# Performance work log

Measured on AMD Instinct MI355X. Metric: run time of the kernel, lower is better.

The kernel has to match this reference:

```python
import jax, jax.numpy as jnp
from jax import lax
import numpy as np

WINDOW_SIZES = (1, 2, 3)


def _proj(x, w1, b1, w2, b2):
    # gated projection: sigmoid(Linear1) * tanh(Linear2)
    return jax.nn.sigmoid(x @ w1.T + b1) * jnp.tanh(x @ w2.T + b2)


def setup_inputs() -> dict:
    key = jax.random.key(0)
    ks = jax.random.split(key, 16)
    V, E, D = 50000, 1024, 1024
    N, La, Lq = 64, 512, 64
    s = 0.02  # weight scale to keep sigmoid/tanh unsaturated
    return {
        "data_q": jax.random.randint(ks[0], (Lq,), 0, V),
        "data_as": jax.random.randint(ks[1], (N, La), 0, V),
        "emb": jax.random.normal(ks[2], (V, E), jnp.float32),
        "w1": jax.random.normal(ks[3], (D, E), jnp.float32) * s,
        "b1": jnp.zeros((D,), jnp.float32),
        "w2": jax.random.normal(ks[4], (D, E), jnp.float32) * s,
        "b2": jnp.zeros((D,), jnp.float32),
        "cw1": jax.random.normal(ks[5], (D, D, 1), jnp.float32) * s,
        "cb1": jnp.zeros((D,), jnp.float32),
        "cw2": jax.random.normal(ks[6], (D, D, 2), jnp.float32) * s,
        "cb2": jnp.zeros((D,), jnp.float32),
        "cw3": jax.random.normal(ks[7], (D, D, 3), jnp.float32) * s,
        "cb3": jnp.zeros((D,), jnp.float32),
        "lin_w": jax.random.normal(ks[8], (D, 3 * D), jnp.float32) * s,
        "lin_b": jnp.zeros((D,), jnp.float32),
        "soft_w": jax.random.normal(ks[9], (1, D), jnp.float32) * s,
        "soft_b": jnp.zeros((1,), jnp.float32),
    }


def reference(data_q, data_as, emb, w1, b1, w2, b2,
              cw1, cb1, cw2, cb2, cw3, cb3, lin_w, lin_b, soft_w, soft_b):
    N, La = data_as.shape
    a_tok = data_as.reshape(-1)                     # [T] concatenated answers
    emb_a = emb[a_tok]                              # [T, E]
    emb_q = emb[data_q]                             # [Lq, E]
    pa = _proj(emb_a, w1, b1, w2, b2)               # [T, D]
    pq = _proj(emb_q, w1, b1, w2, b2)               # [Lq, D]

    # attention: M_r = q @ a^T ; alpha = softmax over question positions
    M = pq @ pa.T                                   # [Lq, T]
    alpha = jax.nn.softmax(M.T, axis=1)             # [T, Lq]
    Y = alpha @ pq                                  # [T, D]
    sim = pa * Y                                    # elementwise compare (mul)

    starts = jnp.arange(N) * La
    x = sim.T[None]                                 # [1, D, T]
    pools = []
    for w, cw, cb in zip(WINDOW_SIZES, (cw1, cw2, cw3), (cb1, cb2, cb3)):
        conv = lax.conv_general_dilated(
            x, cw, (1,), 'VALID',
            dimension_numbers=('NCW', 'OIW', 'NCW'))[0].T + cb  # [T-w+1, D]
        conv = jax.nn.relu(conv)
        # DMax: per-answer max over rows [start_k, start_k + La - w + 1)
        idx = starts[:, None] + jnp.arange(La - w + 1)[None, :]  # [N, La-w+1]
        pools.append(conv[idx].max(axis=1))          # [N, D]

    cat = jnp.concatenate(pools, axis=1)            # [N, 3D]
    h = jnp.tanh(cat @ lin_w.T + lin_b)             # [N, D]
    logits = (h @ soft_w.T + soft_b).reshape(-1)    # [N]
    return jax.nn.log_softmax(logits)
```

## Files before the change

### kernel.cpp

```cpp
#include <hip/hip_runtime.h>

#define DEV __device__ __forceinline__

typedef __bf16 bf16x8 __attribute__((ext_vector_type(8)));
typedef float f32x4 __attribute__((ext_vector_type(4)));
typedef unsigned short u16;
typedef u16 u16x4 __attribute__((ext_vector_type(4)));

constexpr int T_ANS = 32768;
constexpr int LQ    = 64;
constexpr int M_ALL = T_ANS + LQ;
constexpr int M_PAD = 33024;
constexpr int DIM   = 1024;

DEV u16 f2bf(float x) {
  unsigned u = __float_as_uint(x);
  return (u16)((u + 0x7FFFu + ((u >> 16) & 1u)) >> 16);
}
DEV float bf2f(u16 s) { return __uint_as_float(((unsigned)s) << 16); }

DEV void gl2lds16(const void* g, void* l) {
  __builtin_amdgcn_global_load_lds(
      (const __attribute__((address_space(1))) unsigned int*)g,
      (__attribute__((address_space(3))) unsigned int*)l, 16, 0, 0);
}

#define MF(A, B, C) __builtin_amdgcn_mfma_f32_16x16x32_bf16(A, B, C, 0, 0, 0)
#define LFC(P, OFF) (*(const bf16x8*)((P) + (OFF)))


#define STG(G, LT, R0) gl2lds16((G) + (R0) * 2048 + gOff, (LT) + (R0) * 64 + ldOff)

#define S_TILE(AT, BT, BUF)                                                           \
  { const char* ga_ = (AT); const char* gb_ = (BT); char* lb_ = (BUF);                \
    STG(ga_, lb_, 0); STG(ga_, lb_, 128);                                             \
    STG(gb_, lb_ + 16384, 0); STG(gb_, lb_ + 16384, 128); }

#define VMC4 asm volatile("s_waitcnt vmcnt(4)" ::: "memory");
#define VMC0 asm volatile("s_waitcnt vmcnt(0)" ::: "memory");

#define TILEV3(BUF, STAGES, WAIT)                                                     \
  {                                                                                   \
    STAGES                                                                            \
    const char* Ar = (BUF) + rdA;                                                     \
    const char* Br = (BUF) + 16384 + rdB;                                             \
    bf16x8 a0 = LFC(Ar, 0),    a1 = LFC(Ar, 1024), a2 = LFC(Ar, 2048), a3 = LFC(Ar, 3072); \
    bf16x8 a4 = LFC(Ar, 4096), a5 = LFC(Ar, 5120), a6 = LFC(Ar, 6144), a7 = LFC(Ar, 7168); \
    bf16x8 c0 = LFC(Br, 0), c1 = LFC(Br, 1024), c2 = LFC(Br, 2048), c3 = LFC(Br, 3072);    \
    acc[0][0] = MF(a0, c0, acc[0][0]); acc[0][1] = MF(a0, c1, acc[0][1]);             \
    acc[0][2] = MF(a0, c2, acc[0][2]); acc[0][3] = MF(a0, c3, acc[0][3]);             \
    acc[1][0] = MF(a1, c0, acc[1][0]); acc[1][1] = MF(a1, c1, acc[1][1]);             \
    acc[1][2] = MF(a1, c2, acc[1][2]); acc[1][3] = MF(a1, c3, acc[1][3]);             \
    acc[2][0] = MF(a2, c0, acc[2][0]); acc[2][1] = MF(a2, c1, acc[2][1]);             \
    acc[2][2] = MF(a2, c2, acc[2][2]); acc[2][3] = MF(a2, c3, acc[2][3]);             \
    acc[3][0] = MF(a3, c0, acc[3][0]); acc[3][1] = MF(a3, c1, acc[3][1]);             \
    acc[3][2] = MF(a3, c2, acc[3][2]); acc[3][3] = MF(a3, c3, acc[3][3]);             \
    acc[4][0] = MF(a4, c0, acc[4][0]); acc[4][1] = MF(a4, c1, acc[4][1]);             \
    acc[4][2] = MF(a4, c2, acc[4][2]); acc[4][3] = MF(a4, c3, acc[4][3]);             \
    acc[5][0] = MF(a5, c0, acc[5][0]); acc[5][1] = MF(a5, c1, acc[5][1]);             \
    acc[5][2] = MF(a5, c2, acc[5][2]); acc[5][3] = MF(a5, c3, acc[5][3]);             \
    acc[6][0] = MF(a6, c0, acc[6][0]); acc[6][1] = MF(a6, c1, acc[6][1]);             \
    acc[6][2] = MF(a6, c2, acc[6][2]); acc[6][3] = MF(a6, c3, acc[6][3]);             \
    acc[7][0] = MF(a7, c0, acc[7][0]); acc[7][1] = MF(a7, c1, acc[7][1]);             \
    acc[7][2] = MF(a7, c2, acc[7][2]); acc[7][3] = MF(a7, c3, acc[7][3]);             \
    WAIT                                                                              \
    asm volatile("s_barrier" ::: "memory");                                           \
  }

#define CORE_BASES                                                                    \
  const int ldOff = tid * 16;                                                         \
  const int gOff = (tid >> 2) * 2048 + (((tid & 3) ^ ((tid >> 2) & 3)) << 4);         \
  const int blk_ = (((lane >> 4) ^ (lane & 3)) << 4);                                 \
  const int rdA = (wm + (lane & 15)) * 64 + blk_;                                     \
  const int rdB = (wn + (lane & 15)) * 64 + blk_;                                     \
  char* b0_ = lds; char* b1_ = lds + 32768; char* b2_ = lds + 65536; char* b3_ = lds + 98304;

#define GROUP4(T0)                                                                    \
    TILEV3(b0_, S_TILE(Ab((T0) + 2), Bb((T0) + 2), b2_), VMC4)                        \
    TILEV3(b1_, S_TILE(Ab((T0) + 3), Bb((T0) + 3), b3_), VMC4)                        \
    TILEV3(b2_, S_TILE(Ab((T0) + 4), Bb((T0) + 4), b0_), VMC4)                        \
    TILEV3(b3_, S_TILE(Ab((T0) + 5), Bb((T0) + 5), b1_), VMC4)


__global__ __launch_bounds__(256)
void prep_all(const float* __restrict__ w1, const float* __restrict__ w2,
              u16* __restrict__ W12,
              const float* __restrict__ lin_w, u16* __restrict__ linb,
              const float* __restrict__ cw1, const float* __restrict__ cw2,
              const float* __restrict__ cw3, u16* __restrict__ cwb,
              float* __restrict__ cat,
              const int* __restrict__ dq, const int* __restrict__ das,
              const float* __restrict__ emb, u16* __restrict__ X) {
  const int b = blockIdx.x, t = threadIdx.x;
  if (b < 8192) {
    int i = b * 256 + t;
    int n2 = i >> 10, k = i & 1023;
    int j = n2 >> 4, m = n2 & 15;
    const float* src = (j & 1) ? w2 : w1;
    W12[i] = f2bf(src[(size_t)((j >> 1) * 16 + m) * 1024 + k]);
  } else if (b < 11264) {
    int i = (b - 8192) * 256 + t;
    float4 v = ((const float4*)lin_w)[i];
    u16x4 o = { f2bf(v.x), f2bf(v.y), f2bf(v.z), f2bf(v.w) };
    ((u16x4*)linb)[i] = o;
  } else if (b < 23552) {
    int rb = b - 11264;
    int W = 1 + (rb >> 12);
    int i = (rb & 4095) * 256 + t;
    const float* src = (W == 1) ? cw1 : (W == 2) ? cw2 : cw3;
    u16* dst = cwb + ((W == 1) ? 0 : (W == 2) ? (size_t)1 * 1048576 : (size_t)3 * 1048576);
#pragma unroll 3
    for (int k = 0; k < 3; ++k)
      if (k < W)
        dst[(size_t)k * 1048576 + i] = f2bf(src[(size_t)i * W + k]);
  } else if (b < 24320) {
    cat[(b - 23552) * 256 + t] = 0.f;
  } else {
    const int row = b - 24320;
    size_t dsto = (size_t)row * DIM + t * 4;
    if (row >= M_ALL) {
      u16x4 z = {0, 0, 0, 0};
      *(u16x4*)(X + dsto) = z;
      return;
    }
    const int tok = (row < T_ANS) ? das[row] : dq[row - T_ANS];
    float4 v = ((const float4*)(emb + (size_t)tok * DIM))[t];
    u16x4 o = { f2bf(v.x), f2bf(v.y), f2bf(v.z), f2bf(v.w) };
    *(u16x4*)(X + dsto) = o;
  }
}

__global__ void transpose_pq(const u16* __restrict__ pa, u16* __restrict__ pqT) {
  int i = blockIdx.x * 256 + threadIdx.x;
  int e = i >> 6, q = i & 63;
  pqT[i] = pa[(size_t)(T_ANS + q) * DIM + e];
}

__global__ void zero_pad_sim(u16* __restrict__ sim) {
  int i = blockIdx.x * 256 + threadIdx.x;
  if (i < 2 * DIM) sim[(size_t)T_ANS * DIM + i] = 0;
}

__global__ void cast_cat(const float* __restrict__ cat, u16* __restrict__ catb) {
  int i = blockIdx.x * 256 + threadIdx.x;
  if (i < 128 * 3072) {
    int row = i / 3072;
    catb[i] = (row < 64) ? f2bf(cat[i]) : (u16)0;
  }
}


__global__ __launch_bounds__(256)
void proj_g(const u16* __restrict__ X, const u16* __restrict__ W12,
            const float* __restrict__ b1, const float* __restrict__ b2,
            u16* __restrict__ pa) {
  __shared__ alignas(16) u16 sA[128 * 32];
  __shared__ alignas(16) u16 sB[128 * 32];
  const int tid = threadIdx.x, lane = tid & 63;
  const int wid = tid >> 6;
  const int wm = (wid >> 1) * 64, wn = (wid & 1) * 64;
  const int wg = ((int)blockIdx.x % 8) * 516 + (int)blockIdx.x / 8;
  const int tm = (wg >> 4) * 128, tn = (wg & 15) * 128;
  f32x4 acc[4][4] = {};
  for (int k0 = 0; k0 < 1024; k0 += 32) {
#pragma unroll
    for (int j = 0; j < 2; ++j) {
      const int f = tid * 16 + j * 4096;
      const int r = f >> 6, cb = f & 63;
      gl2lds16((const char*)X   + (size_t)(tm + r) * 2048 + k0 * 2 + cb, (char*)sA + f);
      gl2lds16((const char*)W12 + (size_t)(tn + r) * 2048 + k0 * 2 + cb, (char*)sB + f);
    }
    __syncthreads();
    const int lr = lane & 15, lk = (lane >> 4) * 8;
    bf16x8 af[4], bf[4];
#pragma unroll
    for (int i = 0; i < 4; ++i) {
      af[i] = *(const bf16x8*)(sA + (wm + i * 16 + lr) * 32 + lk);
      bf[i] = *(const bf16x8*)(sB + (wn + i * 16 + lr) * 32 + lk);
    }
#pragma unroll
    for (int mi = 0; mi < 4; ++mi)
#pragma unroll
      for (int ni = 0; ni < 4; ++ni)
        acc[mi][ni] = MF(af[mi], bf[ni], acc[mi][ni]);
    __syncthreads();
  }
  const int lr = lane & 15, lg = (lane >> 4) * 4;
#pragma unroll
  for (int np = 0; np < 2; ++np) {
    const int col = ((tn + wn) >> 1) + np * 16 + lr;
    const float b1v = b1[col], b2v = b2[col];
#pragma unroll
    for (int mi = 0; mi < 4; ++mi)
#pragma unroll
      for (int r = 0; r < 4; ++r) {
        const int row = tm + wm + mi * 16 + lg + r;
        const float x1 = acc[mi][2 * np][r] + b1v;
        const float x2 = acc[mi][2 * np + 1][r] + b2v;
        const float sg = 1.f / (1.f + __expf(-x1));
        const float th = 2.f / (1.f + __expf(-2.f * x2)) - 1.f;
        pa[(size_t)row * DIM + col] = f2bf(sg * th);
      }
  }
}


__global__ __launch_bounds__(512, 1)
void conv_fused(const u16* __restrict__ sim, const u16* __restrict__ cwb,
                const float* __restrict__ cb1, const float* __restrict__ cb2,
                const float* __restrict__ cb3, float* __restrict__ cat) {
  extern __shared__ char lds[];
  const int tid = threadIdx.x, lane = tid & 63;
  const int wid = tid >> 6;
  const int wm = (wid >> 2) * 128, wn = (wid & 3) * 64;
  const int lr = lane & 15;
  const int wg = ((int)blockIdx.x % 8) * 64 + (int)blockIdx.x / 8;
  const int tm = (wg >> 2) * 256, tn = (wg & 3) * 256;
  const char* Ag = (const char*)sim + (size_t)tm * 2048;
  const char* Bg = (const char*)cwb + (size_t)tn * 2048;
  auto Ab = [&](int t) {
    const int g = t >> 5;
    const int tap = g - (g > 0) - 2 * (g > 2);
    return Ag + tap * 2048 + ((t & 31) << 6);
  };
  auto Bb = [&](int t) { return Bg + (size_t)(t >> 5) * 2097152 + ((t & 31) << 6); };

  f32x4 acc[8][4] = {};
  CORE_BASES

  const int lg = (lane >> 4) * 4;
  const int n = tm >> 9;
  auto epi = [&](int W, const float* cb, int outoff) {
#pragma unroll
    for (int ni = 0; ni < 4; ++ni) {
      const int col = tn + wn + ni * 16 + lr;
      const float cbv = cb[col];
      float vmax = 0.f;
#pragma unroll
      for (int mi = 0; mi < 8; ++mi)
#pragma unroll
        for (int r = 0; r < 4; ++r) {
          const int t = tm + wm + mi * 16 + lg + r;
          float v = fmaxf(acc[mi][ni][r] + cbv, 0.f);
          if ((t & 511) > 512 - W) v = 0.f;
          vmax = fmaxf(vmax, v);
        }
      vmax = fmaxf(vmax, __shfl_xor(vmax, 16));
      vmax = fmaxf(vmax, __shfl_xor(vmax, 32));
      if (lane < 16)
        atomicMax((int*)&cat[(size_t)n * 3072 + outoff + col], __float_as_int(vmax));
    }
#pragma unroll
    for (int i = 0; i < 8; ++i)
#pragma unroll
      for (int j = 0; j < 4; ++j) acc[i][j] = (f32x4){0.f, 0.f, 0.f, 0.f};
  };

  S_TILE(Ab(0), Bb(0), b0_) S_TILE(Ab(1), Bb(1), b1_)
  VMC4
  asm volatile("s_barrier" ::: "memory");
  for (int g = 0; g < 8; ++g) { GROUP4(4 * g) }
  epi(1, cb1, 0);
  for (int g = 8; g < 24; ++g) { GROUP4(4 * g) }
  epi(2, cb2, 1024);
  for (int g = 24; g < 47; ++g) { GROUP4(4 * g) }
  {
    TILEV3(b0_, S_TILE(Ab(190), Bb(190), b2_), VMC4)
    TILEV3(b1_, S_TILE(Ab(191), Bb(191), b3_), VMC4)
    TILEV3(b2_, , VMC0)
    TILEV3(b3_, , )
  }
  epi(3, cb3, 2048);
}


__global__ __launch_bounds__(256, 2)
void attn_s(const u16* __restrict__ pa, float* __restrict__ Spart) {
  __shared__ alignas(16) u16 sA[128 * 32];
  __shared__ alignas(16) u16 sB[64 * 32];
  const int tid = threadIdx.x, lane = tid & 63;
  const int tm = blockIdx.x * 128;
  const int kbase = blockIdx.y * 256;
  const int wid = tid >> 6;
  const int wm = (wid >> 1) * 64, wn = (wid & 1) * 32;
  const u16* pq = pa + (size_t)T_ANS * DIM;
  f32x4 acc[4][2] = {};
  for (int k0 = kbase; k0 < kbase + 256; k0 += 32) {
#pragma unroll
    for (int j = 0; j < 2; ++j) {
      const int f = tid * 16 + j * 4096;
      const int r = f >> 6, cb = f & 63;
      gl2lds16((const char*)pa + (size_t)(tm + r) * 2048 + k0 * 2 + cb, (char*)sA + f);
    }
    {
      const int f = tid * 16;
      const int r = f >> 6, cb = f & 63;
      gl2lds16((const char*)pq + (size_t)r * 2048 + k0 * 2 + cb, (char*)sB + f);
    }
    __syncthreads();
    const int lr = lane & 15, lk = (lane >> 4) * 8;
    bf16x8 af[4], bfr[2];
#pragma unroll
    for (int i = 0; i < 4; ++i)
      af[i] = *(const bf16x8*)(sA + (wm + i * 16 + lr) * 32 + lk);
#pragma unroll
    for (int i = 0; i < 2; ++i)
      bfr[i] = *(const bf16x8*)(sB + (wn + i * 16 + lr) * 32 + lk);
#pragma unroll
    for (int mi = 0; mi < 4; ++mi)
#pragma unroll
      for (int ni = 0; ni < 2; ++ni)
        acc[mi][ni] = MF(af[mi], bfr[ni], acc[mi][ni]);
    __syncthreads();
  }
  const int lr = lane & 15, lg = (lane >> 4) * 4;
  float* Sp = Spart + (size_t)blockIdx.y * (T_ANS * 64);
#pragma unroll
  for (int mi = 0; mi < 4; ++mi)
#pragma unroll
    for (int ni = 0; ni < 2; ++ni)
#pragma unroll
      for (int r = 0; r < 4; ++r) {
        const int row = tm + wm + mi * 16 + lg + r;
        const int col = wn + ni * 16 + lr;
        Sp[(size_t)row * 64 + col] = acc[mi][ni][r];
      }
}

__global__ void softmax64(const float* __restrict__ Spart, u16* __restrict__ alpha) {
  const int row = blockIdx.x * 4 + (threadIdx.x >> 6);
  const int lane = threadIdx.x & 63;
  const size_t o = (size_t)row * 64 + lane;
  float v = Spart[o] + Spart[(size_t)1 * T_ANS * 64 + o]
          + Spart[(size_t)2 * T_ANS * 64 + o] + Spart[(size_t)3 * T_ANS * 64 + o];
  float m = v;
#pragma unroll
  for (int o2 = 32; o2 > 0; o2 >>= 1) m = fmaxf(m, __shfl_xor(m, o2));
  const float e = __expf(v - m);
  float s = e;
#pragma unroll
  for (int o2 = 32; o2 > 0; o2 >>= 1) s += __shfl_xor(s, o2);
  alpha[(size_t)row * 64 + lane] = f2bf(e / s);
}


__global__ __launch_bounds__(256, 2)
void attn_y_sim(const u16* __restrict__ alpha, const u16* __restrict__ pqT,
                const u16* __restrict__ pa, u16* __restrict__ sim) {
  __shared__ alignas(16) u16 sA[128 * 32];
  __shared__ alignas(16) u16 sB[128 * 32];
  const int tid = threadIdx.x, lane = tid & 63;
  const int tm = blockIdx.x * 128, tn = blockIdx.y * 128;
  const int wid = tid >> 6;
  const int wm = (wid >> 1) * 64, wn = (wid & 1) * 64;
  f32x4 acc[4][4] = {};
  for (int k0 = 0; k0 < 64; k0 += 32) {
#pragma unroll
    for (int j = 0; j < 2; ++j) {
      const int f = tid * 16 + j * 4096;
      const int r = f >> 6, cb = f & 63;
      gl2lds16((const char*)alpha + (size_t)(tm + r) * 128 + k0 * 2 + cb, (char*)sA + f);
      gl2lds16((const char*)pqT   + (size_t)(tn + r) * 128 + k0 * 2 + cb, (char*)sB + f);
    }
    __syncthreads();
    const int lr = lane & 15, lk = (lane >> 4) * 8;
    bf16x8 af[4], bfr[4];
#pragma unroll
    for (int i = 0; i < 4; ++i) {
      af[i]  = *(const bf16x8*)(sA + (wm + i * 16 + lr) * 32 + lk);
      bfr[i] = *(const bf16x8*)(sB + (wn + i * 16 + lr) * 32 + lk);
    }
#pragma unroll
    for (int mi = 0; mi < 4; ++mi)
#pragma unroll
      for (int ni = 0; ni < 4; ++ni)
        acc[mi][ni] = MF(af[mi], bfr[ni], acc[mi][ni]);
    __syncthreads();
  }
  const int lr = lane & 15, lg = (lane >> 4) * 4;
#pragma unroll
  for (int ni = 0; ni < 4; ++ni) {
    const int col = tn + wn + ni * 16 + lr;
#pragma unroll
    for (int mi = 0; mi < 4; ++mi)
#pragma unroll
      for (int r = 0; r < 4; ++r) {
        const int row = tm + wm + mi * 16 + lg + r;
        const size_t o = (size_t)row * DIM + col;
        sim[o] = f2bf(bf2f(pa[o]) * acc[mi][ni][r]);
      }
  }
}


__global__ __launch_bounds__(256, 2)
void final_h(const u16* __restrict__ catb, const u16* __restrict__ linb,
             const float* __restrict__ lin_b, float* __restrict__ h) {
  __shared__ alignas(16) u16 sA[128 * 32];
  __shared__ alignas(16) u16 sB[128 * 32];
  const int tid = threadIdx.x, lane = tid & 63;
  const int tn = blockIdx.y * 128;
  const int wid = tid >> 6;
  const int wm = (wid >> 1) * 64, wn = (wid & 1) * 64;
  f32x4 acc[4][4] = {};
  for (int k0 = 0; k0 < 3072; k0 += 32) {
#pragma unroll
    for (int j = 0; j < 2; ++j) {
      const int f = tid * 16 + j * 4096;
      const int r = f >> 6, cb = f & 63;
      gl2lds16((const char*)catb + (size_t)r * 6144 + k0 * 2 + cb, (char*)sA + f);
      gl2lds16((const char*)linb + (size_t)(tn + r) * 6144 + k0 * 2 + cb, (char*)sB + f);
    }
    __syncthreads();
    const int lr = lane & 15, lk = (lane >> 4) * 8;
    bf16x8 af[4], bfr[4];
#pragma unroll
    for (int i = 0; i < 4; ++i) {
      af[i]  = *(const bf16x8*)(sA + (wm + i * 16 + lr) * 32 + lk);
      bfr[i] = *(const bf16x8*)(sB + (wn + i * 16 + lr) * 32 + lk);
    }
#pragma unroll
    for (int mi = 0; mi < 4; ++mi)
#pragma unroll
      for (int ni = 0; ni < 4; ++ni)
        acc[mi][ni] = MF(af[mi], bfr[ni], acc[mi][ni]);
    __syncthreads();
  }
  const int lr = lane & 15, lg = (lane >> 4) * 4;
#pragma unroll
  for (int ni = 0; ni < 4; ++ni) {
    const int col = tn + wn + ni * 16 + lr;
    const float bv = lin_b[col];
#pragma unroll
    for (int mi = 0; mi < 4; ++mi)
#pragma unroll
      for (int r = 0; r < 4; ++r) {
        const int row = wm + mi * 16 + lg + r;
        if (row < 64) {
          const float x = acc[mi][ni][r] + bv;
          h[(size_t)row * DIM + col] = 2.f / (1.f + __expf(-2.f * x)) - 1.f;
        }
      }
  }
}

__global__ void final_logits(const float* __restrict__ h, const float* __restrict__ soft_w,
                             const float* __restrict__ soft_b, float* __restrict__ out) {
  __shared__ float part[256];
  const int t = threadIdx.x;
  const int n = t >> 2, q = t & 3;
  float s = 0.f;
  for (int j = q * 256; j < q * 256 + 256; ++j) s += h[(size_t)n * DIM + j] * soft_w[j];
  part[t] = s;
  __syncthreads();
  if (t < 64) {
    float logit = part[t * 4] + part[t * 4 + 1] + part[t * 4 + 2] + part[t * 4 + 3] + soft_b[0];
    float m = logit;
#pragma unroll
    for (int o = 32; o > 0; o >>= 1) m = fmaxf(m, __shfl_xor(m, o));
    float e = __expf(logit - m);
    float ssum = e;
#pragma unroll
    for (int o = 32; o > 0; o >>= 1) ssum += __shfl_xor(ssum, o);
    out[t] = (logit - m) - logf(ssum);
  }
}


extern "C" void kernel_launch(void* const* d_in, const int* in_sizes, int n_in,
                              void* d_out, int out_size, void* d_ws, size_t ws_size,
                              hipStream_t stream) {
  const int*   data_q  = (const int*)d_in[0];
  const int*   data_as = (const int*)d_in[1];
  const float* emb     = (const float*)d_in[2];
  const float* w1      = (const float*)d_in[3];
  const float* b1      = (const float*)d_in[4];
  const float* w2      = (const float*)d_in[5];
  const float* b2      = (const float*)d_in[6];
  const float* cw1     = (const float*)d_in[7];
  const float* cb1     = (const float*)d_in[8];
  const float* cw2     = (const float*)d_in[9];
  const float* cb2     = (const float*)d_in[10];
  const float* cw3     = (const float*)d_in[11];
  const float* cb3     = (const float*)d_in[12];
  const float* lin_w   = (const float*)d_in[13];
  const float* lin_b   = (const float*)d_in[14];
  const float* soft_w  = (const float*)d_in[15];
  const float* soft_b  = (const float*)d_in[16];
  float* out = (float*)d_out;

  hipFuncSetAttribute((const void*)conv_fused, hipFuncAttributeMaxDynamicSharedMemorySize, 131072);

  u16* X     = (u16*)d_ws;
  u16* pa    = X    + (size_t)M_PAD * DIM;
  u16* W12   = pa   + (size_t)M_PAD * DIM;
  u16* cwb   = W12  + (size_t)2 * 1024 * 1024;
  u16* linb  = cwb  + (size_t)6 * 1024 * 1024;
  u16* pqT   = linb + (size_t)3 * 1024 * 1024;
  u16* alpha = pqT  + 64 * 1024;
  float* cat = (float*)(alpha + (size_t)T_ANS * 64);
  u16* catb  = (u16*)(cat + 64 * 3072);
  float* h   = (float*)(catb + 128 * 3072);
  u16* simb  = X;
  float* Spart = (float*)X;

  prep_all<<<57344, 256, 0, stream>>>(w1, w2, W12, lin_w, linb, cw1, cw2, cw3, cwb,
                                      cat, data_q, data_as, emb, X);

  proj_g<<<4128, 256, 0, stream>>>(X, W12, b1, b2, pa);
  transpose_pq<<<256, 256, 0, stream>>>(pa, pqT);

  attn_s<<<dim3(T_ANS / 128, 4), 256, 0, stream>>>(pa, Spart);
  softmax64<<<T_ANS / 4, 256, 0, stream>>>(Spart, alpha);
  attn_y_sim<<<dim3(T_ANS / 128, 8), 256, 0, stream>>>(alpha, pqT, pa, simb);
  zero_pad_sim<<<8, 256, 0, stream>>>(simb);

  conv_fused<<<512, 512, 131072, stream>>>(simb, cwb, cb1, cb2, cb3, cat);

  cast_cat<<<1536, 256, 0, stream>>>(cat, catb);
  final_h<<<dim3(1, 8), 256, 0, stream>>>(catb, linb, lin_b, h);
  final_logits<<<1, 256, 0, stream>>>(h, soft_w, soft_b, out);
}
```

Baseline: 736.6 us.

## Rewrite projection GEMM as persistent 256-row tiles with 4-stage LDS pipeline

The gated projection GEMM for answer tokens is rebuilt to reuse the conv kernel's deep pipelined MFMA core. It launches 256 persistent 512-thread blocks that each own 256 rows and sweep four 128-wide column segments (w1 and w2 interleaved), running the sigmoid*tanh epilogue after each segment. The question rows get their own small kernel. The LDS swizzle is also changed, which affects the shared conv kernel too. This is meant to raise MFMA utilization and A-tile reuse over the old 128x128 tile kernel, at the cost of fewer blocks and higher register pressure.

New measurement: 895.4 us. 1.22x slower.

```diff
diff --git a/kernel.cpp b/kernel.cpp
--- a/kernel.cpp
+++ b/kernel.cpp
@@ -69,8 +69,8 @@
 
 #define CORE_BASES                                                                    \
   const int ldOff = tid * 16;                                                         \
-  const int gOff = (tid >> 2) * 2048 + (((tid & 3) ^ ((tid >> 2) & 3)) << 4);         \
-  const int blk_ = (((lane >> 4) ^ (lane & 3)) << 4);                                 \
+  const int gOff = (tid >> 2) * 2048 + (((tid & 3) ^ ((tid >> 3) & 3)) << 4);         \
+  const int blk_ = (((lane >> 4) ^ ((lane >> 1) & 3)) << 4);                          \
   const int rdA = (wm + (lane & 15)) * 64 + blk_;                                     \
   const int rdB = (wn + (lane & 15)) * 64 + blk_;                                     \
   char* b0_ = lds; char* b1_ = lds + 32768; char* b2_ = lds + 65536; char* b3_ = lds + 98304;
@@ -150,17 +150,81 @@
 }
 
 
-__global__ __launch_bounds__(256)
+__global__ __launch_bounds__(512, 1)
 void proj_g(const u16* __restrict__ X, const u16* __restrict__ W12,
             const float* __restrict__ b1, const float* __restrict__ b2,
             u16* __restrict__ pa) {
+  extern __shared__ char lds[];
+  const int tid = threadIdx.x, lane = tid & 63;
+  const int wid = tid >> 6;
+  const int wm = (wid >> 2) * 128, wn = (wid & 3) * 64;
+  const int lr = lane & 15, lg = (lane >> 4) * 4;
+  const int wg = ((int)blockIdx.x % 8) * 32 + (int)blockIdx.x / 8;
+  const int tm = (wg & 127) * 256, tnh = wg >> 7;
+  const char* Ag = (const char*)X + (size_t)tm * 2048;
+  const char* Bg = (const char*)W12 + (size_t)tnh * 2097152;
+  auto Ab = [&](int t) { return Ag + ((t & 31) << 6); };
+  auto Bb = [&](int t) { return Bg + (size_t)(t >> 5) * 524288 + ((t & 31) << 6); };
+
+  f32x4 acc[8][4] = {};
+  CORE_BASES
+
+  auto epi = [&](int seg) {
+    const int colbase = (tnh * 4 + seg) * 128;
+#pragma unroll
+    for (int pp = 0; pp < 2; ++pp) {
+      const int clocal = ((wn >> 5) + pp) * 16 + lr;
+      const int col = colbase + clocal;
+      const float b1v = b1[col], b2v = b2[col];
+#pragma unroll
+      for (int mi = 0; mi < 8; ++mi)
+#pragma unroll
+        for (int r = 0; r < 4; ++r) {
+          const int row = tm + wm + mi * 16 + lg + r;
+          const float x1 = acc[mi][2 * pp][r] + b1v;
+          const float x2 = acc[mi][2 * pp + 1][r] + b2v;
+          const float sg = 1.f / (1.f + __expf(-x1));
+          const float th = 2.f / (1.f + __expf(-2.f * x2)) - 1.f;
+          pa[(size_t)row * DIM + col] = f2bf(sg * th);
+        }
+    }
+#pragma unroll
+    for (int i = 0; i < 8; ++i)
+#pragma unroll
+      for (int j = 0; j < 4; ++j) acc[i][j] = (f32x4){0.f, 0.f, 0.f, 0.f};
+  };
+
+  S_TILE(Ab(0), Bb(0), b0_) S_TILE(Ab(1), Bb(1), b1_)
+  VMC4
+  asm volatile("s_barrier" ::: "memory");
+  for (int g = 0; g < 8; ++g) { GROUP4(4 * g) }
+  epi(0);
+  for (int g = 8; g < 16; ++g) { GROUP4(4 * g) }
+  epi(1);
+  for (int g = 16; g < 24; ++g) { GROUP4(4 * g) }
+  epi(2);
+  for (int g = 24; g < 31; ++g) { GROUP4(4 * g) }
+  {
+    TILEV3(b0_, S_TILE(Ab(126), Bb(126), b2_), VMC4)
+    TILEV3(b1_, S_TILE(Ab(127), Bb(127), b3_), VMC4)
+    TILEV3(b2_, , VMC0)
+    TILEV3(b3_, , )
+  }
+  epi(3);
+}
+
+
+__global__ __launch_bounds__(256)
+void proj_pq(const u16* __restrict__ X, const u16* __restrict__ W12,
+             const float* __restrict__ b1, const float* __restrict__ b2,
+             u16* __restrict__ pa) {
   __shared__ alignas(16) u16 sA[128 * 32];
   __shared__ alignas(16) u16 sB[128 * 32];
   const int tid = threadIdx.x, lane = tid & 63;
   const int wid = tid >> 6;
   const int wm = (wid >> 1) * 64, wn = (wid & 1) * 64;
-  const int wg = ((int)blockIdx.x % 8) * 516 + (int)blockIdx.x / 8;
-  const int tm = (wg >> 4) * 128, tn = (wg & 15) * 128;
+  const int tm = T_ANS;
+  const int tn = (int)blockIdx.x * 128;
   f32x4 acc[4][4] = {};
   for (int k0 = 0; k0 < 1024; k0 += 32) {
 #pragma unroll
@@ -489,6 +553,7 @@
   const float* soft_b  = (const float*)d_in[16];
   float* out = (float*)d_out;
 
+  hipFuncSetAttribute((const void*)proj_g, hipFuncAttributeMaxDynamicSharedMemorySize, 131072);
   hipFuncSetAttribute((const void*)conv_fused, hipFuncAttributeMaxDynamicSharedMemorySize, 131072);
 
   u16* X     = (u16*)d_ws;
@@ -507,7 +572,8 @@
   prep_all<<<57344, 256, 0, stream>>>(w1, w2, W12, lin_w, linb, cw1, cw2, cw3, cwb,
                                       cat, data_q, data_as, emb, X);
 
-  proj_g<<<4128, 256, 0, stream>>>(X, W12, b1, b2, pa);
+  proj_pq<<<16, 256, 0, stream>>>(X, W12, b1, b2, pa);
+  proj_g<<<256, 512, 131072, stream>>>(X, W12, b1, b2, pa);
   transpose_pq<<<256, 256, 0, stream>>>(pa, pqT);
 
   attn_s<<<dim3(T_ANS / 128, 4), 256, 0, stream>>>(pa, Spart);
```
